# Optimization experiments

Measured on AMD Instinct MI355X. Metric: run time of the kernel, lower is better.

## Reference

```python
import jax, jax.numpy as jnp
import numpy as np
from jax import lax

WINDOW = 11
SIGMA = 1.5
CHANNELS = 3
DATA_RANGE = 1.0
WEIGHTS = (0.0448, 0.2856, 0.3001, 0.2363, 0.1333)


def _gaussian_kernel_2d(size, sigma, channels):
    x = np.arange(size, dtype=np.float32) - size // 2
    k1 = np.exp(-x ** 2 / (2 * sigma ** 2))
    k1 = k1 / k1.sum()
    k2 = np.outer(k1, k1)
    k2 = k2 / k2.sum()
    return jnp.asarray(np.tile(k2[None, None], (channels, 1, 1, 1)), dtype=jnp.float32)


def _depthwise_blur(x, kernel):
    # x: [B, G, H, W], kernel: [C, 1, kh, kw] tiled to G groups
    groups = x.shape[1]
    reps = groups // kernel.shape[0]
    k = jnp.tile(kernel, (reps, 1, 1, 1))
    return lax.conv_general_dilated(
        x, k, window_strides=(1, 1), padding='SAME',
        feature_group_count=groups,
        dimension_numbers=('NCHW', 'OIHW', 'NCHW'))


def _avg_pool2(x):
    b, c, h, w = x.shape
    return x.reshape(b, c, h // 2, 2, w // 2, 2).mean(axis=(3, 5))


def _ssim_components(pred, target, kernel):
    C1 = (0.01 * DATA_RANGE) ** 2
    C2 = (0.03 * DATA_RANGE) ** 2
    # Fuse the 5 depthwise blurs into a single grouped conv over stacked channels
    stacked = jnp.concatenate(
        [pred, target, pred * pred, target * target, pred * target], axis=1)
    blurred = _depthwise_blur(stacked, kernel)
    mu1, mu2, e_pp, e_tt, e_pt = jnp.split(blurred, 5, axis=1)
    mu1_sq = mu1 * mu1
    mu2_sq = mu2 * mu2
    mu1_mu2 = mu1 * mu2
    sigma1_sq = jnp.maximum(e_pp - mu1_sq, 0.0)
    sigma2_sq = jnp.maximum(e_tt - mu2_sq, 0.0)
    sigma12 = e_pt - mu1_mu2
    l = (2 * mu1_mu2 + C1) / (mu1_sq + mu2_sq + C1)
    cs = (2 * sigma12 + C2) / (sigma1_sq + sigma2_sq + C2)
    return l.mean(), cs.mean()


def setup_inputs() -> dict:
    key = jax.random.key(0)
    k1, k2 = jax.random.split(key)
    pred = jax.random.uniform(k1, (16, 3, 512, 512), dtype=jnp.float32)
    target = jax.random.uniform(k2, (16, 3, 512, 512), dtype=jnp.float32)
    kernel = _gaussian_kernel_2d(WINDOW, SIGMA, CHANNELS)
    return {'pred': pred, 'target': target, 'kernel': kernel}


def reference(pred, target, kernel):
    weights = jnp.asarray(WEIGHTS, dtype=pred.dtype)
    msssim = jnp.ones((1,), dtype=pred.dtype)
    n_scales = len(WEIGHTS)
    for i in range(n_scales):
        if i > 0:
            pred = _avg_pool2(pred)
            target = _avg_pool2(target)
        if pred.shape[2] < WINDOW or pred.shape[3] < WINDOW:
            break
        l, cs = _ssim_components(pred, target, kernel)
        if i == n_scales - 1:
            msssim = msssim * jnp.maximum(l, 1e-8) ** weights[i] \
                            * jnp.maximum(cs, 1e-8) ** weights[i]
        else:
            msssim = msssim * jnp.maximum(cs, 1e-8) ** weights[i]
    return msssim
```

## Files before the change

### kernel.cpp

```cpp
#include <hip/hip_runtime.h>
#include <math.h>

#define NP 48

typedef float v2f __attribute__((ext_vector_type(2)));

__device__ __forceinline__ float uniform_f(float v) {
    int i = __builtin_amdgcn_readfirstlane(__builtin_bit_cast(int, v));
    return __builtin_bit_cast(float, i);
}

template<bool GT, bool GB>
__device__ __forceinline__ void ssim_loop(
        const float* __restrict__ pP, const float* __restrict__ pT, int H,
        const float* __restrict__ w,
        const float* __restrict__ wc,
        float& lsum, float& csum)
{
    v2f wmu[11], we[11];
    float wpt[11];
    const float C1 = 1e-4f, C2 = 9e-4f;
#pragma unroll
    for (int s = 0; s < 42; ++s) {
        v2f a_mu = (v2f){0.f, 0.f};
        v2f a_e  = (v2f){0.f, 0.f};
        v2f a_pt = (v2f){0.f, 0.f};
        if ((!GT || s >= 5) && (!GB || s < 37)) {
#pragma unroll
            for (int j = 0; j < 11; ++j) {
                v2f pt2 = (v2f){pP[j], pT[j]};
                v2f wv  = (v2f){wc[j], wc[j]};
                v2f wp2 = wv * pt2;
                v2f ptr2 = (v2f){pt2.y, pt2.x};
                a_mu += wp2;
                a_e  += wp2 * pt2;
                a_pt += wp2 * ptr2;
            }
        }
        wmu[s % 11] = a_mu;
        we[s % 11]  = a_e;
        wpt[s % 11] = a_pt.x + a_pt.y;
        if (s >= 10) {
            v2f mu2 = (v2f){0.f, 0.f};
            v2f e2  = (v2f){0.f, 0.f};
            float ept = 0.f;
#pragma unroll
            for (int i = 0; i < 11; ++i) {
                const int sl = (s + 1 + i) % 11;
                v2f wi = (v2f){w[i], w[i]};
                mu2 += wi * wmu[sl];
                e2  += wi * we[sl];
                ept += w[i] * wpt[sl];
            }
            float m11 = mu2.x * mu2.x, m22 = mu2.y * mu2.y, m12 = mu2.x * mu2.y;
            float s1  = fmaxf(e2.x - m11, 0.f);
            float s2  = fmaxf(e2.y - m22, 0.f);
            float s12 = 0.5f * ept - m12;
            lsum += (2.f * m12 + C1) * __builtin_amdgcn_rcpf(m11 + m22 + C1);
            csum += (2.f * s12 + C2) * __builtin_amdgcn_rcpf(s1 + s2 + C2);
        }
        pP += H; pT += H;
    }
}

__device__ __forceinline__ void ssim_scale(
        const float* __restrict__ P, const float* __restrict__ T,
        int H, int sh, int lb, int scale, int slotsel, int tid,
        const float* __restrict__ k2d, double* __restrict__ accum)
{
    float w[11];
    {
        float s = 0.f;
#pragma unroll
        for (int i = 0; i < 11; ++i) s += k2d[55 + i];
        float inv = 1.0f / s;
#pragma unroll
        for (int i = 0; i < 11; ++i) w[i] = uniform_f(k2d[55 + i] * inv);
    }

    int blocksX = (NP << sh) >> 8;
    int bxi = lb % blocksX;
    int by  = lb / blocksX;
    int g   = (bxi << 8) + tid;
    int pl  = g >> sh;
    int x   = g & (H - 1);
    int yb  = by * 32;

    int bcl = x - 5;
    bcl = bcl < 0 ? 0 : bcl;
    bcl = bcl > H - 11 ? H - 11 : bcl;
    int d = bcl - (x - 5);
    float wc[11];
#pragma unroll
    for (int j = 0; j < 11; ++j) {
        int idx = j + d;
        float val = 0.f;
#pragma unroll
        for (int i = 0; i < 11; ++i) val = (idx == i) ? w[i] : val;
        wc[j] = val;
    }

    const float* pP = P + (size_t)pl * H * H + (ptrdiff_t)(yb - 5) * H + bcl;
    const float* pT = T + (size_t)pl * H * H + (ptrdiff_t)(yb - 5) * H + bcl;

    float lsum = 0.f, csum = 0.f;
    bool gt = (yb == 0);
    bool gb = (yb + 32 == H);
    if (gt) {
        if (gb) ssim_loop<true, true >(pP, pT, H, w, wc, lsum, csum);
        else    ssim_loop<true, false>(pP, pT, H, w, wc, lsum, csum);
    } else {
        if (gb) ssim_loop<false, true >(pP, pT, H, w, wc, lsum, csum);
        else    ssim_loop<false, false>(pP, pT, H, w, wc, lsum, csum);
    }

#pragma unroll
    for (int o = 32; o > 0; o >>= 1) {
        lsum += __shfl_down(lsum, o, 64);
        csum += __shfl_down(csum, o, 64);
    }
    __shared__ float red[8];
    int wv = tid >> 6;
    if ((tid & 63) == 0) { red[2 * wv] = lsum; red[2 * wv + 1] = csum; }
    __syncthreads();
    if (tid == 0) {
        int slot = (scale * 8 + slotsel) * 2;
        atomicAdd(&accum[slot],     (double)(red[0] + red[2] + red[4] + red[6]));
        atomicAdd(&accum[slot + 1], (double)(red[1] + red[3] + red[5] + red[7]));
    }
}

__global__ __launch_bounds__(256) void k_main(
        const float* __restrict__ pred, const float* __restrict__ targ,
        float* __restrict__ p1, float* __restrict__ t1,
        float* __restrict__ p2, float* __restrict__ t2,
        float* __restrict__ p3, float* __restrict__ t3,
        float* __restrict__ p4, float* __restrict__ t4,
        const float* __restrict__ k2d, double* __restrict__ accum) {
    int b   = blockIdx.x;
    int tid = threadIdx.x;
    if (b >= 1536) {
        ssim_scale(pred, targ, 512, 9, b - 1536, 0, b & 7, tid, k2d, accum);
        return;
    }
    int pi   = b >> 4;
    int tile = b & 15;
    int pls  = pi < 48 ? pi : pi - 48;
    const float* src = (pi < 48 ? pred : targ) + (size_t)pls * 512 * 512;
    float* d1 = (pi < 48 ? p1 : t1) + (size_t)pls * 256 * 256;
    float* d2 = (pi < 48 ? p2 : t2) + (size_t)pls * 128 * 128;
    float* d3 = (pi < 48 ? p3 : t3) + (size_t)pls * 64 * 64;
    float* d4 = (pi < 48 ? p4 : t4) + (size_t)pls * 32 * 32;
    int tY = tile >> 2, tX = tile & 3;
    int ty = tid >> 4, tx = tid & 15;
    int gy0 = tY * 128 + ty * 8, gx0 = tX * 128 + tx * 8;

    float s1v[4][4];
#pragma unroll
    for (int i = 0; i < 4; ++i) {
        const float* r0 = src + (size_t)(gy0 + 2 * i) * 512 + gx0;
        const float* r1 = r0 + 512;
        float4 a0 = *(const float4*)r0, a1 = *(const float4*)(r0 + 4);
        float4 b0 = *(const float4*)r1, b1 = *(const float4*)(r1 + 4);
        s1v[i][0] = 0.25f * ((a0.x + a0.y) + (b0.x + b0.y));
        s1v[i][1] = 0.25f * ((a0.z + a0.w) + (b0.z + b0.w));
        s1v[i][2] = 0.25f * ((a1.x + a1.y) + (b1.x + b1.y));
        s1v[i][3] = 0.25f * ((a1.z + a1.w) + (b1.z + b1.w));
        *(float4*)(d1 + (size_t)(tY * 64 + ty * 4 + i) * 256 + tX * 64 + tx * 4) =
            *(float4*)s1v[i];
    }
    float s2v[2][2];
#pragma unroll
    for (int i = 0; i < 2; ++i) {
#pragma unroll
        for (int j = 0; j < 2; ++j)
            s2v[i][j] = 0.25f * ((s1v[2*i][2*j] + s1v[2*i][2*j+1]) +
                                 (s1v[2*i+1][2*j] + s1v[2*i+1][2*j+1]));
        *(float2*)(d2 + (size_t)(tY * 32 + ty * 2 + i) * 128 + tX * 32 + tx * 2) =
            *(float2*)s2v[i];
    }
    float s3 = 0.25f * ((s2v[0][0] + s2v[0][1]) + (s2v[1][0] + s2v[1][1]));
    d3[(size_t)(tY * 16 + ty) * 64 + tX * 16 + tx] = s3;
    float v1 = s3 + __shfl_xor(s3, 1, 64);
    float v2 = v1 + __shfl_xor(v1, 16, 64);
    if ((ty & 1) == 0 && (tx & 1) == 0)
        d4[(size_t)(tY * 8 + (ty >> 1)) * 32 + tX * 8 + (tx >> 1)] = 0.25f * v2;
}

__global__ __launch_bounds__(256) void k_ssim_rest(
        const float* __restrict__ p1, const float* __restrict__ t1,
        const float* __restrict__ p2, const float* __restrict__ t2,
        const float* __restrict__ p3, const float* __restrict__ t3,
        const float* __restrict__ p4, const float* __restrict__ t4,
        const float* __restrict__ k2d, double* __restrict__ accum) {
    int b   = blockIdx.x;
    int tid = threadIdx.x;
    if (b < 384)      ssim_scale(p1, t1, 256, 8, b,       1, b & 7, tid, k2d, accum);
    else if (b < 480) ssim_scale(p2, t2, 128, 7, b - 384, 2, b & 7, tid, k2d, accum);
    else if (b < 504) ssim_scale(p3, t3, 64,  6, b - 480, 3, b & 7, tid, k2d, accum);
    else              ssim_scale(p4, t4, 32,  5, b - 504, 4, b & 7, tid, k2d, accum);
}

__global__ void k_final(const double* __restrict__ accum, float* __restrict__ out) {
    if (threadIdx.x != 0 || blockIdx.x != 0) return;
    const float wts[5] = {0.0448f, 0.2856f, 0.3001f, 0.2363f, 0.1333f};
    float ms = 1.0f;
    int Hs = 512;
    for (int s = 0; s < 5; ++s) {
        double lt = 0.0, ct = 0.0;
        for (int k = 0; k < 8; ++k) {
            lt += accum[(s * 8 + k) * 2];
            ct += accum[(s * 8 + k) * 2 + 1];
        }
        float N  = 48.0f * (float)Hs * (float)Hs;
        float l  = (float)lt / N;
        float cs = (float)ct / N;
        cs = fmaxf(cs, 1e-8f);
        if (s == 4) {
            l = fmaxf(l, 1e-8f);
            ms *= powf(l, wts[s]) * powf(cs, wts[s]);
        } else {
            ms *= powf(cs, wts[s]);
        }
        Hs >>= 1;
    }
    out[0] = ms;
}

extern "C" void kernel_launch(void* const* d_in, const int* in_sizes, int n_in,
                              void* d_out, int out_size, void* d_ws, size_t ws_size,
                              hipStream_t stream) {
    const float* pred = (const float*)d_in[0];
    const float* targ = (const float*)d_in[1];
    const float* kern = (const float*)d_in[2];
    float* out = (float*)d_out;

    char* ws = (char*)d_ws;
    double* accum = (double*)ws;
    size_t off = 1024;
    float* p1 = (float*)(ws + off); off += (size_t)NP * 256 * 256 * 4;
    float* t1 = (float*)(ws + off); off += (size_t)NP * 256 * 256 * 4;
    float* p2 = (float*)(ws + off); off += (size_t)NP * 128 * 128 * 4;
    float* t2 = (float*)(ws + off); off += (size_t)NP * 128 * 128 * 4;
    float* p3 = (float*)(ws + off); off += (size_t)NP * 64 * 64 * 4;
    float* t3 = (float*)(ws + off); off += (size_t)NP * 64 * 64 * 4;
    float* p4 = (float*)(ws + off); off += (size_t)NP * 32 * 32 * 4;
    float* t4 = (float*)(ws + off); off += (size_t)NP * 32 * 32 * 4;

    hipMemsetAsync(accum, 0, 640, stream);
    k_main<<<3072, 256, 0, stream>>>(pred, targ, p1, t1, p2, t2, p3, t3, p4, t4, kern, accum);
    k_ssim_rest<<<510, 256, 0, stream>>>(p1, t1, p2, t2, p3, t3, p4, t4, kern, accum);
    k_final<<<1, 1, 0, stream>>>(accum, out);
}
```

Measured before the change: 231.0 us.

## Fuse pooling, all SSIM scales and final reduction into one kernel

Merges the pooling/scale-0 kernel, the lower-scale SSIM kernel and the final combine into a single launch. Blocks for the lower scales spin on a global counter until all pooling blocks finish, and the last block to finish, detected via an atomic done counter, computes the final MS-SSIM value. The row loop is also rewritten from a fully unrolled 42-step template into a 4x11 chunked loop with runtime boundary checks. This aims to remove launch gaps and tail idle time between kernels. In exchange it adds spin-waiting that depends on blocks being scheduled in order, plus runtime branches in the inner loop.

```diff
diff --git a/kernel.cpp b/kernel.cpp
--- a/kernel.cpp
+++ b/kernel.cpp
@@ -10,63 +10,11 @@
     return __builtin_bit_cast(float, i);
 }
 
-template<bool GT, bool GB>
-__device__ __forceinline__ void ssim_loop(
-        const float* __restrict__ pP, const float* __restrict__ pT, int H,
-        const float* __restrict__ w,
-        const float* __restrict__ wc,
-        float& lsum, float& csum)
-{
-    v2f wmu[11], we[11];
-    float wpt[11];
-    const float C1 = 1e-4f, C2 = 9e-4f;
-#pragma unroll
-    for (int s = 0; s < 42; ++s) {
-        v2f a_mu = (v2f){0.f, 0.f};
-        v2f a_e  = (v2f){0.f, 0.f};
-        v2f a_pt = (v2f){0.f, 0.f};
-        if ((!GT || s >= 5) && (!GB || s < 37)) {
-#pragma unroll
-            for (int j = 0; j < 11; ++j) {
-                v2f pt2 = (v2f){pP[j], pT[j]};
-                v2f wv  = (v2f){wc[j], wc[j]};
-                v2f wp2 = wv * pt2;
-                v2f ptr2 = (v2f){pt2.y, pt2.x};
-                a_mu += wp2;
-                a_e  += wp2 * pt2;
-                a_pt += wp2 * ptr2;
-            }
-        }
-        wmu[s % 11] = a_mu;
-        we[s % 11]  = a_e;
-        wpt[s % 11] = a_pt.x + a_pt.y;
-        if (s >= 10) {
-            v2f mu2 = (v2f){0.f, 0.f};
-            v2f e2  = (v2f){0.f, 0.f};
-            float ept = 0.f;
-#pragma unroll
-            for (int i = 0; i < 11; ++i) {
-                const int sl = (s + 1 + i) % 11;
-                v2f wi = (v2f){w[i], w[i]};
-                mu2 += wi * wmu[sl];
-                e2  += wi * we[sl];
-                ept += w[i] * wpt[sl];
-            }
-            float m11 = mu2.x * mu2.x, m22 = mu2.y * mu2.y, m12 = mu2.x * mu2.y;
-            float s1  = fmaxf(e2.x - m11, 0.f);
-            float s2  = fmaxf(e2.y - m22, 0.f);
-            float s12 = 0.5f * ept - m12;
-            lsum += (2.f * m12 + C1) * __builtin_amdgcn_rcpf(m11 + m22 + C1);
-            csum += (2.f * s12 + C2) * __builtin_amdgcn_rcpf(s1 + s2 + C2);
-        }
-        pP += H; pT += H;
-    }
-}
-
 __device__ __forceinline__ void ssim_scale(
         const float* __restrict__ P, const float* __restrict__ T,
         int H, int sh, int lb, int scale, int slotsel, int tid,
-        const float* __restrict__ k2d, double* __restrict__ accum)
+        const float* __restrict__ k2d, double* __restrict__ accum,
+        unsigned* __restrict__ done, float* __restrict__ out)
 {
     float w[11];
     {
@@ -85,6 +33,7 @@
     int pl  = g >> sh;
     int x   = g & (H - 1);
     int yb  = by * 32;
+    int yend = yb + 32;
 
     int bcl = x - 5;
     bcl = bcl < 0 ? 0 : bcl;
@@ -103,15 +52,54 @@
     const float* pP = P + (size_t)pl * H * H + (ptrdiff_t)(yb - 5) * H + bcl;
     const float* pT = T + (size_t)pl * H * H + (ptrdiff_t)(yb - 5) * H + bcl;
 
+    v2f wmu[11], we[11];
+    float wpt[11];
+    const float C1 = 1e-4f, C2 = 9e-4f;
     float lsum = 0.f, csum = 0.f;
-    bool gt = (yb == 0);
-    bool gb = (yb + 32 == H);
-    if (gt) {
-        if (gb) ssim_loop<true, true >(pP, pT, H, w, wc, lsum, csum);
-        else    ssim_loop<true, false>(pP, pT, H, w, wc, lsum, csum);
-    } else {
-        if (gb) ssim_loop<false, true >(pP, pT, H, w, wc, lsum, csum);
-        else    ssim_loop<false, false>(pP, pT, H, w, wc, lsum, csum);
+    int rr = yb - 5;
+
+    for (int ch = 0; ch < 4; ++ch) {
+#pragma unroll
+        for (int ph = 0; ph < 11; ++ph) {
+            bool live = rr < yend + 5;
+            v2f a_mu = (v2f){0.f, 0.f};
+            v2f a_e  = (v2f){0.f, 0.f};
+            v2f a_pt = (v2f){0.f, 0.f};
+            if (live && rr >= 0 && rr < H) {
+#pragma unroll
+                for (int j = 0; j < 11; ++j) {
+                    v2f pt2 = (v2f){pP[j], pT[j]};
+                    v2f wv  = (v2f){wc[j], wc[j]};
+                    v2f wp2 = wv * pt2;
+                    v2f ptr2 = (v2f){pt2.y, pt2.x};
+                    a_mu += wp2;
+                    a_e  += wp2 * pt2;
+                    a_pt += wp2 * ptr2;
+                }
+            }
+            wmu[ph] = a_mu; we[ph] = a_e;
+            wpt[ph] = a_pt.x + a_pt.y;
+            if (live && rr >= yb + 5) {
+                v2f mu2 = (v2f){0.f, 0.f};
+                v2f e2  = (v2f){0.f, 0.f};
+                float ept = 0.f;
+#pragma unroll
+                for (int i = 0; i < 11; ++i) {
+                    const int sl = (ph + 1 + i) % 11;
+                    v2f wi = (v2f){w[i], w[i]};
+                    mu2 += wi * wmu[sl];
+                    e2  += wi * we[sl];
+                    ept += w[i] * wpt[sl];
+                }
+                float m11 = mu2.x * mu2.x, m22 = mu2.y * mu2.y, m12 = mu2.x * mu2.y;
+                float s1  = fmaxf(e2.x - m11, 0.f);
+                float s2  = fmaxf(e2.y - m22, 0.f);
+                float s12 = 0.5f * ept - m12;
+                lsum += (2.f * m12 + C1) * __builtin_amdgcn_rcpf(m11 + m22 + C1);
+                csum += (2.f * s12 + C2) * __builtin_amdgcn_rcpf(s1 + s2 + C2);
+            }
+            rr++; pP += H; pT += H;
+        }
     }
 
 #pragma unroll
@@ -127,104 +115,112 @@
         int slot = (scale * 8 + slotsel) * 2;
         atomicAdd(&accum[slot],     (double)(red[0] + red[2] + red[4] + red[6]));
         atomicAdd(&accum[slot + 1], (double)(red[1] + red[3] + red[5] + red[7]));
-    }
-}
-
-__global__ __launch_bounds__(256) void k_main(
+        __threadfence();
+        unsigned old = atomicAdd(done, 1u);
+        if (old == 2045u) {
+            __threadfence();
+            const float wts[5] = {0.0448f, 0.2856f, 0.3001f, 0.2363f, 0.1333f};
+            float ms = 1.0f;
+            int Hs = 512;
+            for (int s = 0; s < 5; ++s) {
+                double lt = 0.0, ct = 0.0;
+                for (int k = 0; k < 8; ++k) {
+                    lt += atomicAdd(&accum[(s * 8 + k) * 2],     0.0);
+                    ct += atomicAdd(&accum[(s * 8 + k) * 2 + 1], 0.0);
+                }
+                float N  = 48.0f * (float)Hs * (float)Hs;
+                float l  = (float)lt / N;
+                float cs = fmaxf((float)ct / N, 1e-8f);
+                if (s == 4) {
+                    l = fmaxf(l, 1e-8f);
+                    ms *= powf(l, wts[s]) * powf(cs, wts[s]);
+                } else {
+                    ms *= powf(cs, wts[s]);
+                }
+                Hs >>= 1;
+            }
+            out[0] = ms;
+        }
+    }
+}
+
+__global__ __launch_bounds__(256) void k_fused(
         const float* __restrict__ pred, const float* __restrict__ targ,
         float* __restrict__ p1, float* __restrict__ t1,
         float* __restrict__ p2, float* __restrict__ t2,
         float* __restrict__ p3, float* __restrict__ t3,
         float* __restrict__ p4, float* __restrict__ t4,
-        const float* __restrict__ k2d, double* __restrict__ accum) {
+        const float* __restrict__ k2d, double* __restrict__ accum,
+        unsigned* __restrict__ poolcnt, unsigned* __restrict__ done,
+        float* __restrict__ out) {
     int b   = blockIdx.x;
     int tid = threadIdx.x;
-    if (b >= 1536) {
-        ssim_scale(pred, targ, 512, 9, b - 1536, 0, b & 7, tid, k2d, accum);
+
+    if (b < 1536) {
+        int pi   = b >> 4;
+        int tile = b & 15;
+        int pls  = pi < 48 ? pi : pi - 48;
+        const float* src = (pi < 48 ? pred : targ) + (size_t)pls * 512 * 512;
+        float* d1 = (pi < 48 ? p1 : t1) + (size_t)pls * 256 * 256;
+        float* d2 = (pi < 48 ? p2 : t2) + (size_t)pls * 128 * 128;
+        float* d3 = (pi < 48 ? p3 : t3) + (size_t)pls * 64 * 64;
+        float* d4 = (pi < 48 ? p4 : t4) + (size_t)pls * 32 * 32;
+        int tY = tile >> 2, tX = tile & 3;
+        int ty = tid >> 4, tx = tid & 15;
+        int gy0 = tY * 128 + ty * 8, gx0 = tX * 128 + tx * 8;
+
+        float s1v[4][4];
+#pragma unroll
+        for (int i = 0; i < 4; ++i) {
+            const float* r0 = src + (size_t)(gy0 + 2 * i) * 512 + gx0;
+            const float* r1 = r0 + 512;
+            float4 a0 = *(const float4*)r0, a1 = *(const float4*)(r0 + 4);
+            float4 b0 = *(const float4*)r1, b1 = *(const float4*)(r1 + 4);
+            s1v[i][0] = 0.25f * ((a0.x + a0.y) + (b0.x + b0.y));
+            s1v[i][1] = 0.25f * ((a0.z + a0.w) + (b0.z + b0.w));
+            s1v[i][2] = 0.25f * ((a1.x + a1.y) + (b1.x + b1.y));
+            s1v[i][3] = 0.25f * ((a1.z + a1.w) + (b1.z + b1.w));
+            *(float4*)(d1 + (size_t)(tY * 64 + ty * 4 + i) * 256 + tX * 64 + tx * 4) =
+                *(float4*)s1v[i];
+        }
+        float s2v[2][2];
+#pragma unroll
+        for (int i = 0; i < 2; ++i) {
+#pragma unroll
+            for (int j = 0; j < 2; ++j)
+                s2v[i][j] = 0.25f * ((s1v[2*i][2*j] + s1v[2*i][2*j+1]) +
+                                     (s1v[2*i+1][2*j] + s1v[2*i+1][2*j+1]));
+            *(float2*)(d2 + (size_t)(tY * 32 + ty * 2 + i) * 128 + tX * 32 + tx * 2) =
+                *(float2*)s2v[i];
+        }
+        float s3 = 0.25f * ((s2v[0][0] + s2v[0][1]) + (s2v[1][0] + s2v[1][1]));
+        d3[(size_t)(tY * 16 + ty) * 64 + tX * 16 + tx] = s3;
+        float v1 = s3 + __shfl_xor(s3, 1, 64);
+        float v2 = v1 + __shfl_xor(v1, 16, 64);
+        if ((ty & 1) == 0 && (tx & 1) == 0)
+            d4[(size_t)(tY * 8 + (ty >> 1)) * 32 + tX * 8 + (tx >> 1)] = 0.25f * v2;
+        __threadfence();
+        __syncthreads();
+        if (tid == 0) atomicAdd(poolcnt, 1u);
         return;
     }
-    int pi   = b >> 4;
-    int tile = b & 15;
-    int pls  = pi < 48 ? pi : pi - 48;
-    const float* src = (pi < 48 ? pred : targ) + (size_t)pls * 512 * 512;
-    float* d1 = (pi < 48 ? p1 : t1) + (size_t)pls * 256 * 256;
-    float* d2 = (pi < 48 ? p2 : t2) + (size_t)pls * 128 * 128;
-    float* d3 = (pi < 48 ? p3 : t3) + (size_t)pls * 64 * 64;
-    float* d4 = (pi < 48 ? p4 : t4) + (size_t)pls * 32 * 32;
-    int tY = tile >> 2, tX = tile & 3;
-    int ty = tid >> 4, tx = tid & 15;
-    int gy0 = tY * 128 + ty * 8, gx0 = tX * 128 + tx * 8;
-
-    float s1v[4][4];
-#pragma unroll
-    for (int i = 0; i < 4; ++i) {
-        const float* r0 = src + (size_t)(gy0 + 2 * i) * 512 + gx0;
-        const float* r1 = r0 + 512;
-        float4 a0 = *(const float4*)r0, a1 = *(const float4*)(r0 + 4);
-        float4 b0 = *(const float4*)r1, b1 = *(const float4*)(r1 + 4);
-        s1v[i][0] = 0.25f * ((a0.x + a0.y) + (b0.x + b0.y));
-        s1v[i][1] = 0.25f * ((a0.z + a0.w) + (b0.z + b0.w));
-        s1v[i][2] = 0.25f * ((a1.x + a1.y) + (b1.x + b1.y));
-        s1v[i][3] = 0.25f * ((a1.z + a1.w) + (b1.z + b1.w));
-        *(float4*)(d1 + (size_t)(tY * 64 + ty * 4 + i) * 256 + tX * 64 + tx * 4) =
-            *(float4*)s1v[i];
-    }
-    float s2v[2][2];
-#pragma unroll
-    for (int i = 0; i < 2; ++i) {
-#pragma unroll
-        for (int j = 0; j < 2; ++j)
-            s2v[i][j] = 0.25f * ((s1v[2*i][2*j] + s1v[2*i][2*j+1]) +
-                                 (s1v[2*i+1][2*j] + s1v[2*i+1][2*j+1]));
-        *(float2*)(d2 + (size_t)(tY * 32 + ty * 2 + i) * 128 + tX * 32 + tx * 2) =
-            *(float2*)s2v[i];
-    }
-    float s3 = 0.25f * ((s2v[0][0] + s2v[0][1]) + (s2v[1][0] + s2v[1][1]));
-    d3[(size_t)(tY * 16 + ty) * 64 + tX * 16 + tx] = s3;
-    float v1 = s3 + __shfl_xor(s3, 1, 64);
-    float v2 = v1 + __shfl_xor(v1, 16, 64);
-    if ((ty & 1) == 0 && (tx & 1) == 0)
-        d4[(size_t)(tY * 8 + (ty >> 1)) * 32 + tX * 8 + (tx >> 1)] = 0.25f * v2;
-}
-
-__global__ __launch_bounds__(256) void k_ssim_rest(
-        const float* __restrict__ p1, const float* __restrict__ t1,
-        const float* __restrict__ p2, const float* __restrict__ t2,
-        const float* __restrict__ p3, const float* __restrict__ t3,
-        const float* __restrict__ p4, const float* __restrict__ t4,
-        const float* __restrict__ k2d, double* __restrict__ accum) {
-    int b   = blockIdx.x;
-    int tid = threadIdx.x;
-    if (b < 384)      ssim_scale(p1, t1, 256, 8, b,       1, b & 7, tid, k2d, accum);
-    else if (b < 480) ssim_scale(p2, t2, 128, 7, b - 384, 2, b & 7, tid, k2d, accum);
-    else if (b < 504) ssim_scale(p3, t3, 64,  6, b - 480, 3, b & 7, tid, k2d, accum);
-    else              ssim_scale(p4, t4, 32,  5, b - 504, 4, b & 7, tid, k2d, accum);
-}
-
-__global__ void k_final(const double* __restrict__ accum, float* __restrict__ out) {
-    if (threadIdx.x != 0 || blockIdx.x != 0) return;
-    const float wts[5] = {0.0448f, 0.2856f, 0.3001f, 0.2363f, 0.1333f};
-    float ms = 1.0f;
-    int Hs = 512;
-    for (int s = 0; s < 5; ++s) {
-        double lt = 0.0, ct = 0.0;
-        for (int k = 0; k < 8; ++k) {
-            lt += accum[(s * 8 + k) * 2];
-            ct += accum[(s * 8 + k) * 2 + 1];
-        }
-        float N  = 48.0f * (float)Hs * (float)Hs;
-        float l  = (float)lt / N;
-        float cs = (float)ct / N;
-        cs = fmaxf(cs, 1e-8f);
-        if (s == 4) {
-            l = fmaxf(l, 1e-8f);
-            ms *= powf(l, wts[s]) * powf(cs, wts[s]);
-        } else {
-            ms *= powf(cs, wts[s]);
-        }
-        Hs >>= 1;
-    }
-    out[0] = ms;
+
+    if (b < 3072) {
+        ssim_scale(pred, targ, 512, 9, b - 1536, 0, b & 7, tid, k2d, accum, done, out);
+        return;
+    }
+
+    if (tid == 0) {
+        while (atomicAdd(poolcnt, 0u) < 1536u) __builtin_amdgcn_s_sleep(8);
+    }
+    __syncthreads();
+    __threadfence();
+
+    int lb = b - 3072;
+    if (lb < 384)      ssim_scale(p1, t1, 256, 8, lb,       1, b & 7, tid, k2d, accum, done, out);
+    else if (lb < 480) ssim_scale(p2, t2, 128, 7, lb - 384, 2, b & 7, tid, k2d, accum, done, out);
+    else if (lb < 504) ssim_scale(p3, t3, 64,  6, lb - 480, 3, b & 7, tid, k2d, accum, done, out);
+    else               ssim_scale(p4, t4, 32,  5, lb - 504, 4, b & 7, tid, k2d, accum, done, out);
 }
 
 extern "C" void kernel_launch(void* const* d_in, const int* in_sizes, int n_in,
@@ -236,7 +232,9 @@
     float* out = (float*)d_out;
 
     char* ws = (char*)d_ws;
-    double* accum = (double*)ws;
+    double*   accum   = (double*)ws;
+    unsigned* poolcnt = (unsigned*)(ws + 768);
+    unsigned* done    = (unsigned*)(ws + 832);
     size_t off = 1024;
     float* p1 = (float*)(ws + off); off += (size_t)NP * 256 * 256 * 4;
     float* t1 = (float*)(ws + off); off += (size_t)NP * 256 * 256 * 4;
@@ -247,8 +245,7 @@
     float* p4 = (float*)(ws + off); off += (size_t)NP * 32 * 32 * 4;
     float* t4 = (float*)(ws + off); off += (size_t)NP * 32 * 32 * 4;
 
-    hipMemsetAsync(accum, 0, 640, stream);
-    k_main<<<3072, 256, 0, stream>>>(pred, targ, p1, t1, p2, t2, p3, t3, p4, t4, kern, accum);
-    k_ssim_rest<<<510, 256, 0, stream>>>(p1, t1, p2, t2, p3, t3, p4, t4, kern, accum);
-    k_final<<<1, 1, 0, stream>>>(accum, out);
-}
+    hipMemsetAsync(ws, 0, 1024, stream);
+    k_fused<<<3582, 256, 0, stream>>>(pred, targ, p1, t1, p2, t2, p3, t3, p4, t4,
+                                      kern, accum, poolcnt, done, out);
+}
```

Measured after the change: 597.1 us. +158.5%, slower.
